# Optimization experiments

Measured on AMD Instinct MI355X. Metric: run time of the kernel, lower is better.

## Reference

```python
import jax, jax.numpy as jnp
import numpy as np

SEQ, BSZ = 512, 128
VOC, EMB, HDIM = 50000, 128, 256
TAGS = 7
BOS, EOS, PAD = 4, 5, 6
H = HDIM // 2  # per-direction hidden size
NEG = -10000.0


def setup_inputs() -> dict:
    key = jax.random.key(0)
    ks = jax.random.split(key, 12)
    s = 0.08  # ~ pytorch default init scale for these sizes
    trans = jax.random.normal(ks[10], (TAGS, TAGS), dtype=jnp.float32)
    # constraints applied in __init__: no transition FROM BOS targets / INTO EOS etc.
    trans = trans.at[BOS, :].set(NEG).at[:, EOS].set(NEG).at[PAD, :].set(0.0)
    return {
        "sen": jax.random.randint(ks[0], (SEQ, BSZ), 0, VOC),                # (S, B) token ids
        "emb": jax.random.normal(ks[1], (VOC, EMB), jnp.float32) * s,        # embedding table
        "Wih_f": jax.random.normal(ks[2], (4 * H, EMB), jnp.float32) * s,    # fwd dir, gates i,f,g,o
        "Whh_f": jax.random.normal(ks[3], (4 * H, H), jnp.float32) * s,
        "b_f": jax.random.normal(ks[4], (4 * H,), jnp.float32) * s,          # b_ih + b_hh fused
        "Wih_b": jax.random.normal(ks[5], (4 * H, EMB), jnp.float32) * s,    # bwd dir
        "Whh_b": jax.random.normal(ks[6], (4 * H, H), jnp.float32) * s,
        "b_b": jax.random.normal(ks[7], (4 * H,), jnp.float32) * s,
        "W_out": jax.random.normal(ks[8], (TAGS, HDIM), jnp.float32) * s,    # hid2tag
        "b_out": jax.random.normal(ks[9], (TAGS,), jnp.float32) * s,
        "trans": trans,                                                      # trans[next, prev]
    }


def _lstm_dir(x, Wih, Whh, b, reverse):
    """Single-direction LSTM over (S, B, E) -> (S, B, H). PyTorch gate order i,f,g,o."""
    xw = jnp.einsum('sbe,ge->sbg', x, Wih) + b  # hoist input projection out of scan

    def step(carry, xt):
        h, c = carry
        g = xt + h @ Whh.T
        i, f, gg, o = jnp.split(g, 4, axis=-1)
        c = jax.nn.sigmoid(f) * c + jax.nn.sigmoid(i) * jnp.tanh(gg)
        h = jax.nn.sigmoid(o) * jnp.tanh(c)
        return (h, c), h

    B = x.shape[1]
    h0 = jnp.zeros((B, H), x.dtype)
    _, hs = jax.lax.scan(step, (h0, h0), xw, reverse=reverse)
    return hs


def reference(sen, emb, Wih_f, Whh_f, b_f, Wih_b, Whh_b, b_b, W_out, b_out, trans):
    # ----- BiLSTM features -----
    x = emb[sen]                                   # (S, B, E)
    hf = _lstm_dir(x, Wih_f, Whh_f, b_f, reverse=False)
    hb = _lstm_dir(x, Wih_b, Whh_b, b_b, reverse=True)
    fts = jnp.concatenate([hf, hb], axis=-1) @ W_out.T + b_out   # (S, B, TAGS)

    # ----- Viterbi decode (batched, one scan over sequence) -----
    B = fts.shape[1]
    fv0 = jnp.full((B, TAGS), NEG, dtype=fts.dtype).at[:, BOS].set(0.0)

    def vstep(fv, ft):
        # scores[b, next, prev] = fv[b, prev] + trans[next, prev]
        scores = fv[:, None, :] + trans[None, :, :]
        bptr = jnp.argmax(scores, axis=2)          # (B, TAGS) best prev per next tag
        fv_new = jnp.max(scores, axis=2) + ft
        return fv_new, bptr

    fv, bptrs = jax.lax.scan(vstep, fv0, fts)      # bptrs: (S, B, TAGS)
    terminal = fv + trans[EOS]                     # (B, TAGS)
    best = jnp.argmax(terminal, axis=1)            # (B,)
    path_score = jnp.take_along_axis(terminal, best[:, None], axis=1)[:, 0]

    def bstep(cur, bptr):
        prev = jnp.take_along_axis(bptr, cur[:, None], axis=1)[:, 0]
        return prev, cur                           # output = tag at this position

    _, tag_seq = jax.lax.scan(bstep, best, bptrs, reverse=True)  # (S, B)
    return path_score, tag_seq
```

## Files before the change

### kernel.cpp

```cpp
#include <hip/hip_runtime.h>
#include <hip/hip_bf16.h>
#include <math.h>

#define SEQ  512
#define BSZ  128
#define EMBD 128
#define H4   512
#define HD   128
#define NTAG 7
#define BOSX 4
#define EOSX 5
#define NEGC (-10000.0f)

typedef _Float16 h2 __attribute__((ext_vector_type(2)));
typedef _Float16 f16x8 __attribute__((ext_vector_type(8)));
typedef float    f32x4 __attribute__((ext_vector_type(4)));

__device__ __forceinline__ float frcp(float x) { return __builtin_amdgcn_rcpf(x); }

__device__ __forceinline__ float fdot2(h2 a, h2 b, float c) {
#if __has_builtin(__builtin_amdgcn_fdot2)
    return __builtin_amdgcn_fdot2(a, b, c, false);
#else
    return c + (float)a.x * (float)b.x + (float)a.y * (float)b.y;
#endif
}

template<int C> __device__ __forceinline__ float dppaddf(float x) {
    const int y = __builtin_amdgcn_update_dpp(0, __builtin_bit_cast(int, x), C, 0xF, 0xF, true);
    return x + __builtin_bit_cast(float, y);
}
template<int C> __device__ __forceinline__ float dppmovf(float x) {
    return __builtin_bit_cast(float,
        __builtin_amdgcn_update_dpp(0, __builtin_bit_cast(int, x), C, 0xF, 0xF, true));
}
template<int C> __device__ __forceinline__ int dppmovi(int x) {
    return __builtin_amdgcn_update_dpp(0, x, C, 0xF, 0xF, true);
}
__device__ __forceinline__ float kreduce4(float x) {
    x = dppaddf<0xB1>(x);
    x = dppaddf<0x4E>(x);
    return x;
}

#define CH_DW  20
#define ROW_DW 80

__device__ __forceinline__ float dot32h(const h2* __restrict__ w, const h2* __restrict__ x) {
    float a = 0.f;
    #pragma unroll
    for (int j = 0; j < 16; ++j) a = fdot2(w[j], x[j], a);
    return a;
}
__device__ __forceinline__ void ldwh(h2* w, const float4* wr) {
    #pragma unroll
    for (int j = 0; j < 8; ++j) {
        const float4 f4 = wr[j];
        h2 a; a.x = (_Float16)f4.x; a.y = (_Float16)f4.y;
        h2 b; b.x = (_Float16)f4.z; b.y = (_Float16)f4.w;
        w[2 * j] = a; w[2 * j + 1] = b;
    }
}
__device__ __forceinline__ void unp16(const uint4* p, h2* x) {
    #pragma unroll
    for (int j = 0; j < 4; ++j) {
        x[4 * j]     = __builtin_bit_cast(h2, p[j].x);
        x[4 * j + 1] = __builtin_bit_cast(h2, p[j].y);
        x[4 * j + 2] = __builtin_bit_cast(h2, p[j].z);
        x[4 * j + 3] = __builtin_bit_cast(h2, p[j].w);
    }
}

__global__ __launch_bounds__(512) __attribute__((amdgpu_waves_per_eu(1, 2)))
void bilstm_fused(const int* __restrict__ sen, const float* __restrict__ emb,
                  const float* __restrict__ Wih_f, const float* __restrict__ b_f,
                  const float* __restrict__ Wih_b, const float* __restrict__ b_b,
                  const float* __restrict__ Whh_f, const float* __restrict__ Whh_b,
                  const float* __restrict__ W_out,
                  float* __restrict__ eft, float* __restrict__ ebt)
{
    const int tid = threadIdx.x;
    const int wid = tid >> 6;
    const int lane = tid & 63;
    const int k = lane & 3;
    const int m = lane >> 2;
    const int u = wid * 16 + m;
    const bool bk0 = (lane & 1) != 0;
    const bool bk1 = (lane & 2) != 0;
    const int col = lane & 15;
    const int kg  = lane >> 4;
    const int chain = blockIdx.x;
    const int dir = chain & 1;
    const int b = chain >> 1;
    const int t0 = dir ? (SEQ - 1) : 0;
    const int ts = dir ? -1 : 1;

    __shared__ __align__(16) _Float16 xA[2][4][4][16][8];
    __shared__ __align__(16) float zb[2][8][512];
    __shared__ __align__(16) unsigned hdb_u[2 * ROW_DW];

    const float* __restrict__ Wih  = dir ? Wih_b : Wih_f;
    const float* __restrict__ Whh  = dir ? Whh_b : Whh_f;
    const float* __restrict__ bias = dir ? b_b  : b_f;

    h2 whh[4][16], wo[16];
    #pragma unroll
    for (int g = 0; g < 4; ++g)
        ldwh(whh[g], (const float4*)(Whh + (g * HD + u) * HD + k * 32));
    {
        const int mm = (m < NTAG) ? m : 0;
        ldwh(wo, (const float4*)(W_out + mm * 256 + dir * HD + k * 32));
    }
    f16x8 bw[4][4];
    float biasv[4];
    #pragma unroll
    for (int tt = 0; tt < 4; ++tt) {
        const int R = (wid * 4 + tt) * 16 + col;
        const int ug = R >> 2;
        const int gg = R & 3;
        #pragma unroll
        for (int ks = 0; ks < 4; ++ks) {
            const float* src = Wih + (gg * HD + ug) * EMBD + ks * 32 + kg * 8;
            f16x8 v;
            #pragma unroll
            for (int j = 0; j < 8; ++j) v[j] = (_Float16)src[j];
            bw[tt][ks] = v;
        }
        biasv[tt] = bias[gg * HD + ug];
    }

    if (tid < 2 * ROW_DW) hdb_u[tid] = 0u;
    {
        unsigned* p = (unsigned*)xA;
        p[tid] = 0u; p[tid + 512] = 0u; p[tid + 1024] = 0u; p[tid + 1536] = 0u;
    }

    const int srow = wid;
    const int sp = lane;
    float2 sv;
    auto sissue = [&](int w) {
        const int row = w * 8 + srow;
        const int tg = t0 + ts * row;
        const int tok = sen[tg * BSZ + b];
        sv = *(const float2*)(emb + (size_t)tok * EMBD + 2 * sp);
    };
    auto swrite = [&](int buf) {
        h2 t; t.x = (_Float16)sv.x; t.y = (_Float16)sv.y;
        *(unsigned*)&xA[buf][sp >> 4][(sp >> 2) & 3][srow][(sp & 3) * 2]
            = __builtin_bit_cast(unsigned, t);
    };

    auto proj = [&](int bufp, int nb) {
        f16x8 ax[4];
        #pragma unroll
        for (int ks = 0; ks < 4; ++ks)
            ax[ks] = *(const f16x8*)&xA[bufp][ks][kg][col][0];
        f32x4 acc[4];
        #pragma unroll
        for (int tt = 0; tt < 4; ++tt) { acc[tt][0]=0.f; acc[tt][1]=0.f; acc[tt][2]=0.f; acc[tt][3]=0.f; }
        #pragma unroll
        for (int ks = 0; ks < 4; ++ks)
            #pragma unroll
            for (int tt = 0; tt < 4; ++tt)
                acc[tt] = __builtin_amdgcn_mfma_f32_16x16x32_f16(ax[ks], bw[tt][ks], acc[tt], 0, 0, 0);
        if (lane < 32) {
            #pragma unroll
            for (int tt = 0; tt < 4; ++tt)
                #pragma unroll
                for (int r = 0; r < 4; ++r)
                    zb[nb][(lane >> 4) * 4 + r][wid * 64 + tt * 16 + col]
                        = acc[tt][r] + biasv[tt];
        }
    };

    float c = 0.0f, v0 = 0.0f, v1 = 0.0f, v2 = 0.0f, v3 = 0.0f;
    float* __restrict__ eX = (dir ? ebt : eft) + (size_t)b * (SEQ * 8);

    sissue(0); swrite(0);
    sissue(1); swrite(1);
    __syncthreads();
    proj(0, 0);
    sissue(2);
    __syncthreads();

    for (int base = 0; base < SEQ; base += 8) {
        const int W = base >> 3;
        #pragma unroll
        for (int sl = 0; sl < 8; ++sl) {
            const int s = base + sl;
            const int cur = sl & 1;
            uint4 hpk[4];
            {
                const uint4* hr = (const uint4*)(hdb_u + cur * ROW_DW + k * CH_DW);
                #pragma unroll
                for (int j = 0; j < 4; ++j) hpk[j] = hr[j];
            }
            if (sl == 0) {
                if (base <= SEQ - 24) swrite(W & 1);
                if (base <= SEQ - 32) sissue(W + 3);
                if (W < 63) proj((W & 1) ^ 1, (W & 1) ^ 1);
            }
            const float xq = zb[W & 1][sl][wid * 64 + lane];
            h2 hx[16];
            unp16(hpk, hx);
            {
                const float pi = dot32h(whh[0], hx);
                const float pf = dot32h(whh[1], hx);
                const float pg = dot32h(whh[2], hx);
                const float po = dot32h(whh[3], hx);
                const float A = (bk0 ? pf : pi) + dppmovf<0xB1>(bk0 ? pi : pf);
                const float B = (bk0 ? po : pg) + dppmovf<0x4E>(bk0 ? pg : po);
                float z = (bk1 ? B : A) + dppmovf<0x4E>(bk1 ? A : B);
                z += xq;
                const bool isg = bk1 && !bk0;
                const float x2 = isg ? (z + z) : z;
                float y = frcp(1.0f + __expf(-x2));
                y = isg ? (2.0f * y - 1.0f) : y;
                const float r1 = dppmovf<0xB1>(y);
                const float r2 = dppmovf<0x4E>(y);
                const float r3 = dppmovf<0x4E>(r1);
                const float i0 = bk0 ? r1 : y,  i1 = bk0 ? y : r1;
                const float i2 = bk0 ? r3 : r2, i3 = bk0 ? r2 : r3;
                const float gi = bk1 ? i2 : i0;
                const float gf = bk1 ? i3 : i1;
                const float gg2 = bk1 ? i0 : i2;
                const float go = bk1 ? i1 : i3;
                c = gf * c + gi * gg2;
                const float th = 2.0f * frcp(1.0f + __expf(-2.0f * c)) - 1.0f;
                const float h = go * th;
                if (k == 0) {
                    ((unsigned short*)hdb_u)[((cur ^ 1) * ROW_DW + (u >> 5) * CH_DW) * 2 + (u & 31)]
                        = __builtin_bit_cast(unsigned short, (_Float16)h);
                }
            }
            if (wid == 0 && s >= 1) {
                const float ev = kreduce4(dot32h(wo, hx));
                const int e = s - 1;
                const bool mine = (e & 3) == k;
                const int j = (e >> 2) & 3;
                v0 = (mine && j == 0) ? ev : v0;
                v1 = (mine && j == 1) ? ev : v1;
                v2 = (mine && j == 2) ? ev : v2;
                v3 = (mine && j == 3) ? ev : v3;
                if ((s & 15) == 0 && m < NTAG) {
                    const int eA = s - 16 + k;
                    eX[(t0 + ts * (eA +  0)) * 8 + m] = v0;
                    eX[(t0 + ts * (eA +  4)) * 8 + m] = v1;
                    eX[(t0 + ts * (eA +  8)) * 8 + m] = v2;
                    eX[(t0 + ts * (eA + 12)) * 8 + m] = v3;
                }
            }
            __syncthreads();
        }
    }

    {
        h2 hx[16];
        const uint4* hr = (const uint4*)(hdb_u + k * CH_DW);
        uint4 pk[4];
        #pragma unroll
        for (int j = 0; j < 4; ++j) pk[j] = hr[j];
        unp16(pk, hx);
        if (wid == 0) {
            const float ev = kreduce4(dot32h(wo, hx));
            if (k == 3) v3 = ev;
            if (m < NTAG) {
                const int eA = SEQ - 16 + k;
                eX[(t0 + ts * (eA +  0)) * 8 + m] = v0;
                eX[(t0 + ts * (eA +  4)) * 8 + m] = v1;
                eX[(t0 + ts * (eA +  8)) * 8 + m] = v2;
                eX[(t0 + ts * (eA + 12)) * 8 + m] = v3;
            }
        }
    }
}

__global__ __launch_bounds__(256, 1)
void vit_kernel(const float* __restrict__ eft, const float* __restrict__ ebt,
                const float* __restrict__ b_out, const float* __restrict__ trans,
                float* __restrict__ out)
{
    const int b = blockIdx.x;
    const int tid = threadIdx.x;
    __shared__ __align__(16) float ftl[SEQ * 8];
    __shared__ unsigned wordL[SEQ];

    {
        const float4* sf = (const float4*)(eft + (size_t)b * (SEQ * 8));
        const float4* sb = (const float4*)(ebt + (size_t)b * (SEQ * 8));
        float4* dst = (float4*)ftl;
        #pragma unroll
        for (int i = 0; i < SEQ * 2 / 256; ++i) {
            const int idx = tid + i * 256;
            float4 a = sf[idx];
            const float4 c4 = sb[idx];
            a.x += c4.x; a.y += c4.y; a.z += c4.z; a.w += c4.w;
            dst[idx] = a;
        }
    }
    __syncthreads();

    if (tid < 64) {
        const int lane = tid;
        const int next = lane >> 3;
        const int prev = lane & 7;
        const bool pv = (prev < NTAG);
        const bool nv = (next < NTAG);
        const float trv = (pv && nv) ? (trans[next * NTAG + prev] + b_out[next]) : -3.0e38f;
        float fvp = pv ? ((prev == BOSX) ? 0.0f : NEGC) : -3.0e38f;

        for (int t = 0; t < SEQ; ++t) {
            float mv = fvp + trv;
            int am = prev;
            {
                const float om = dppmovf<0xB1>(mv); const int oa = dppmovi<0xB1>(am);
                if (om > mv || (om == mv && oa < am)) { mv = om; am = oa; }
            }
            {
                const float om = dppmovf<0x4E>(mv); const int oa = dppmovi<0x4E>(am);
                if (om > mv || (om == mv && oa < am)) { mv = om; am = oa; }
            }
            {
                const float om = dppmovf<0x141>(mv); const int oa = dppmovi<0x141>(am);
                if (om > mv || (om == mv && oa < am)) { mv = om; am = oa; }
            }
            const float fvnew = mv + ftl[t * 8 + next];
            const float nfv = __shfl(fvnew, (lane & 7) << 3);
            const int   amg = __shfl(am,    (lane & 7) << 3);
            unsigned pw = (unsigned)amg << (3 * prev);
            pw |= (unsigned)dppmovi<0xB1>((int)pw);
            pw |= (unsigned)dppmovi<0x4E>((int)pw);
            pw |= (unsigned)dppmovi<0x141>((int)pw);
            if (lane == 0) wordL[t] = pw;
            fvp = pv ? nfv : -3.0e38f;
        }

        float term = pv ? (fvp + trans[EOSX * NTAG + prev]) : -3.0e38f;
        int am = prev;
        {
            const float om = dppmovf<0xB1>(term); const int oa = dppmovi<0xB1>(am);
            if (om > term || (om == term && oa < am)) { term = om; am = oa; }
        }
        {
            const float om = dppmovf<0x4E>(term); const int oa = dppmovi<0x4E>(am);
            if (om > term || (om == term && oa < am)) { term = om; am = oa; }
        }
        {
            const float om = dppmovf<0x141>(term); const int oa = dppmovi<0x141>(am);
            if (om > term || (om == term && oa < am)) { term = om; am = oa; }
        }
        if (lane == 0) out[b] = term;

        unsigned wd[8];
        #pragma unroll
        for (int c2 = 0; c2 < 8; ++c2) wd[c2] = wordL[c2 * 64 + lane];
        int cur = __builtin_amdgcn_readfirstlane(am);
        unsigned pr[8];
        #pragma unroll
        for (int c2 = 7; c2 >= 0; --c2) {
            unsigned acc = 0u;
            for (int tt = 63; tt >= 0; --tt) {
                acc = (lane == tt) ? (unsigned)cur : acc;
                const unsigned w = (unsigned)__builtin_amdgcn_readlane((int)wd[c2], tt);
                cur = (int)((w >> (3 * cur)) & 7u);
            }
            pr[c2] = acc;
        }
        #pragma unroll
        for (int c2 = 0; c2 < 8; ++c2)
            out[BSZ + (c2 * 64 + lane) * BSZ + b] = (float)pr[c2];
    }
}

extern "C" void kernel_launch(void* const* d_in, const int* in_sizes, int n_in,
                              void* d_out, int out_size, void* d_ws, size_t ws_size,
                              hipStream_t stream)
{
    const int*   sen   = (const int*)d_in[0];
    const float* emb   = (const float*)d_in[1];
    const float* Wih_f = (const float*)d_in[2];
    const float* Whh_f = (const float*)d_in[3];
    const float* b_f   = (const float*)d_in[4];
    const float* Wih_b = (const float*)d_in[5];
    const float* Whh_b = (const float*)d_in[6];
    const float* b_b   = (const float*)d_in[7];
    const float* W_out = (const float*)d_in[8];
    const float* b_out = (const float*)d_in[9];
    const float* trans = (const float*)d_in[10];
    float* out = (float*)d_out;

    char* ws = (char*)d_ws;
    const size_t ft_bytes = (size_t)BSZ * SEQ * 8 * 4;
    float* eft = (float*)ws;
    float* ebt = (float*)(ws + ft_bytes);

    bilstm_fused<<<dim3(2 * BSZ), dim3(512), 0, stream>>>(
        sen, emb, Wih_f, b_f, Wih_b, b_b, Whh_f, Whh_b, W_out, eft, ebt);
    vit_kernel<<<dim3(BSZ), dim3(256), 0, stream>>>(eft, ebt, b_out, trans, out);
}
```

Before: 554.8 us.

## Compute LSTM recurrent matvec and emission projection with MFMA instead of fdot2

The per-step h·Whh product moves from per-lane packed fp16 dot products with DPP reductions to 16x16x32 fp16 MFMA. The weights are held as B fragments in the same layout as the input projection, and h is broadcast as the A operand. The tag emission projection also becomes an MFMA on wave 7, and each step's emission is written directly instead of buffered over 16 steps. The aim is to cut the VALU instruction count and cross-lane reduction latency on the serial recurrence. The cost is that 15 of the 16 MFMA rows are redundant, and the critical path now depends on dependent MFMA latency.

```diff
diff --git a/kernel.cpp b/kernel.cpp
--- a/kernel.cpp
+++ b/kernel.cpp
@@ -18,57 +18,12 @@
 
 __device__ __forceinline__ float frcp(float x) { return __builtin_amdgcn_rcpf(x); }
 
-__device__ __forceinline__ float fdot2(h2 a, h2 b, float c) {
-#if __has_builtin(__builtin_amdgcn_fdot2)
-    return __builtin_amdgcn_fdot2(a, b, c, false);
-#else
-    return c + (float)a.x * (float)b.x + (float)a.y * (float)b.y;
-#endif
-}
-
-template<int C> __device__ __forceinline__ float dppaddf(float x) {
-    const int y = __builtin_amdgcn_update_dpp(0, __builtin_bit_cast(int, x), C, 0xF, 0xF, true);
-    return x + __builtin_bit_cast(float, y);
-}
 template<int C> __device__ __forceinline__ float dppmovf(float x) {
     return __builtin_bit_cast(float,
         __builtin_amdgcn_update_dpp(0, __builtin_bit_cast(int, x), C, 0xF, 0xF, true));
 }
 template<int C> __device__ __forceinline__ int dppmovi(int x) {
     return __builtin_amdgcn_update_dpp(0, x, C, 0xF, 0xF, true);
-}
-__device__ __forceinline__ float kreduce4(float x) {
-    x = dppaddf<0xB1>(x);
-    x = dppaddf<0x4E>(x);
-    return x;
-}
-
-#define CH_DW  20
-#define ROW_DW 80
-
-__device__ __forceinline__ float dot32h(const h2* __restrict__ w, const h2* __restrict__ x) {
-    float a = 0.f;
-    #pragma unroll
-    for (int j = 0; j < 16; ++j) a = fdot2(w[j], x[j], a);
-    return a;
-}
-__device__ __forceinline__ void ldwh(h2* w, const float4* wr) {
-    #pragma unroll
-    for (int j = 0; j < 8; ++j) {
-        const float4 f4 = wr[j];
-        h2 a; a.x = (_Float16)f4.x; a.y = (_Float16)f4.y;
-        h2 b; b.x = (_Float16)f4.z; b.y = (_Float16)f4.w;
-        w[2 * j] = a; w[2 * j + 1] = b;
-    }
-}
-__device__ __forceinline__ void unp16(const uint4* p, h2* x) {
-    #pragma unroll
-    for (int j = 0; j < 4; ++j) {
-        x[4 * j]     = __builtin_bit_cast(h2, p[j].x);
-        x[4 * j + 1] = __builtin_bit_cast(h2, p[j].y);
-        x[4 * j + 2] = __builtin_bit_cast(h2, p[j].z);
-        x[4 * j + 3] = __builtin_bit_cast(h2, p[j].w);
-    }
 }
 
 __global__ __launch_bounds__(512) __attribute__((amdgpu_waves_per_eu(1, 2)))
@@ -82,13 +37,10 @@
     const int tid = threadIdx.x;
     const int wid = tid >> 6;
     const int lane = tid & 63;
-    const int k = lane & 3;
-    const int m = lane >> 2;
-    const int u = wid * 16 + m;
+    const int col = lane & 15;
+    const int kg  = lane >> 4;
     const bool bk0 = (lane & 1) != 0;
     const bool bk1 = (lane & 2) != 0;
-    const int col = lane & 15;
-    const int kg  = lane >> 4;
     const int chain = blockIdx.x;
     const int dir = chain & 1;
     const int b = chain >> 1;
@@ -97,21 +49,13 @@
 
     __shared__ __align__(16) _Float16 xA[2][4][4][16][8];
     __shared__ __align__(16) float zb[2][8][512];
-    __shared__ __align__(16) unsigned hdb_u[2 * ROW_DW];
+    __shared__ __align__(16) _Float16 hA[2][128];
 
     const float* __restrict__ Wih  = dir ? Wih_b : Wih_f;
     const float* __restrict__ Whh  = dir ? Whh_b : Whh_f;
     const float* __restrict__ bias = dir ? b_b  : b_f;
 
-    h2 whh[4][16], wo[16];
-    #pragma unroll
-    for (int g = 0; g < 4; ++g)
-        ldwh(whh[g], (const float4*)(Whh + (g * HD + u) * HD + k * 32));
-    {
-        const int mm = (m < NTAG) ? m : 0;
-        ldwh(wo, (const float4*)(W_out + mm * 256 + dir * HD + k * 32));
-    }
-    f16x8 bw[4][4];
+    f16x8 bw[4][4], bwh[4][4], be[4];
     float biasv[4];
     #pragma unroll
     for (int tt = 0; tt < 4; ++tt) {
@@ -120,16 +64,26 @@
         const int gg = R & 3;
         #pragma unroll
         for (int ks = 0; ks < 4; ++ks) {
-            const float* src = Wih + (gg * HD + ug) * EMBD + ks * 32 + kg * 8;
-            f16x8 v;
-            #pragma unroll
-            for (int j = 0; j < 8; ++j) v[j] = (_Float16)src[j];
-            bw[tt][ks] = v;
+            const float* s1 = Wih + (gg * HD + ug) * EMBD + ks * 32 + kg * 8;
+            const float* s2 = Whh + (gg * HD + ug) * HD   + ks * 32 + kg * 8;
+            f16x8 v1, v2;
+            #pragma unroll
+            for (int j = 0; j < 8; ++j) { v1[j] = (_Float16)s1[j]; v2[j] = (_Float16)s2[j]; }
+            bw[tt][ks] = v1; bwh[tt][ks] = v2;
         }
         biasv[tt] = bias[gg * HD + ug];
     }
-
-    if (tid < 2 * ROW_DW) hdb_u[tid] = 0u;
+    #pragma unroll
+    for (int ks = 0; ks < 4; ++ks) {
+        f16x8 v;
+        #pragma unroll
+        for (int j = 0; j < 8; ++j)
+            v[j] = (col < NTAG) ? (_Float16)W_out[col * 256 + dir * HD + ks * 32 + kg * 8 + j]
+                                : (_Float16)0.f;
+        be[ks] = v;
+    }
+
+    if (tid < 256) ((_Float16*)hA)[tid] = (_Float16)0.f;
     {
         unsigned* p = (unsigned*)xA;
         p[tid] = 0u; p[tid + 512] = 0u; p[tid + 1024] = 0u; p[tid + 1536] = 0u;
@@ -173,7 +127,7 @@
         }
     };
 
-    float c = 0.0f, v0 = 0.0f, v1 = 0.0f, v2 = 0.0f, v3 = 0.0f;
+    float c = 0.0f;
     float* __restrict__ eX = (dir ? ebt : eft) + (size_t)b * (SEQ * 8);
 
     sissue(0); swrite(0);
@@ -189,89 +143,68 @@
         for (int sl = 0; sl < 8; ++sl) {
             const int s = base + sl;
             const int cur = sl & 1;
-            uint4 hpk[4];
-            {
-                const uint4* hr = (const uint4*)(hdb_u + cur * ROW_DW + k * CH_DW);
-                #pragma unroll
-                for (int j = 0; j < 4; ++j) hpk[j] = hr[j];
-            }
+            f16x8 ah[4];
+            #pragma unroll
+            for (int ks = 0; ks < 4; ++ks)
+                ah[ks] = *(const f16x8*)&hA[cur][ks * 32 + kg * 8];
             if (sl == 0) {
                 if (base <= SEQ - 24) swrite(W & 1);
                 if (base <= SEQ - 32) sissue(W + 3);
                 if (W < 63) proj((W & 1) ^ 1, (W & 1) ^ 1);
             }
-            const float xq = zb[W & 1][sl][wid * 64 + lane];
-            h2 hx[16];
-            unp16(hpk, hx);
-            {
-                const float pi = dot32h(whh[0], hx);
-                const float pf = dot32h(whh[1], hx);
-                const float pg = dot32h(whh[2], hx);
-                const float po = dot32h(whh[3], hx);
-                const float A = (bk0 ? pf : pi) + dppmovf<0xB1>(bk0 ? pi : pf);
-                const float B = (bk0 ? po : pg) + dppmovf<0x4E>(bk0 ? pg : po);
-                float z = (bk1 ? B : A) + dppmovf<0x4E>(bk1 ? A : B);
-                z += xq;
-                const bool isg = bk1 && !bk0;
+            f32x4 acc[4];
+            #pragma unroll
+            for (int tt = 0; tt < 4; ++tt) { acc[tt][0]=0.f; acc[tt][1]=0.f; acc[tt][2]=0.f; acc[tt][3]=0.f; }
+            #pragma unroll
+            for (int ks = 0; ks < 4; ++ks)
+                #pragma unroll
+                for (int tt = 0; tt < 4; ++tt)
+                    acc[tt] = __builtin_amdgcn_mfma_f32_16x16x32_f16(ah[ks], bwh[tt][ks], acc[tt], 0, 0, 0);
+            f32x4 eacc; eacc[0]=0.f; eacc[1]=0.f; eacc[2]=0.f; eacc[3]=0.f;
+            if (wid == 7 && s >= 1) {
+                #pragma unroll
+                for (int ks = 0; ks < 4; ++ks)
+                    eacc = __builtin_amdgcn_mfma_f32_16x16x32_f16(ah[ks], be[ks], eacc, 0, 0, 0);
+            }
+            const bool isg = bk1 && !bk0;
+            float y[4];
+            #pragma unroll
+            for (int tt = 0; tt < 4; ++tt) {
+                const float z = acc[tt][0] + zb[W & 1][sl][wid * 64 + tt * 16 + col];
                 const float x2 = isg ? (z + z) : z;
-                float y = frcp(1.0f + __expf(-x2));
-                y = isg ? (2.0f * y - 1.0f) : y;
-                const float r1 = dppmovf<0xB1>(y);
-                const float r2 = dppmovf<0x4E>(y);
-                const float r3 = dppmovf<0x4E>(r1);
-                const float i0 = bk0 ? r1 : y,  i1 = bk0 ? y : r1;
-                const float i2 = bk0 ? r3 : r2, i3 = bk0 ? r2 : r3;
-                const float gi = bk1 ? i2 : i0;
-                const float gf = bk1 ? i3 : i1;
-                const float gg2 = bk1 ? i0 : i2;
-                const float go = bk1 ? i1 : i3;
-                c = gf * c + gi * gg2;
-                const float th = 2.0f * frcp(1.0f + __expf(-2.0f * c)) - 1.0f;
-                const float h = go * th;
-                if (k == 0) {
-                    ((unsigned short*)hdb_u)[((cur ^ 1) * ROW_DW + (u >> 5) * CH_DW) * 2 + (u & 31)]
-                        = __builtin_bit_cast(unsigned short, (_Float16)h);
-                }
-            }
-            if (wid == 0 && s >= 1) {
-                const float ev = kreduce4(dot32h(wo, hx));
-                const int e = s - 1;
-                const bool mine = (e & 3) == k;
-                const int j = (e >> 2) & 3;
-                v0 = (mine && j == 0) ? ev : v0;
-                v1 = (mine && j == 1) ? ev : v1;
-                v2 = (mine && j == 2) ? ev : v2;
-                v3 = (mine && j == 3) ? ev : v3;
-                if ((s & 15) == 0 && m < NTAG) {
-                    const int eA = s - 16 + k;
-                    eX[(t0 + ts * (eA +  0)) * 8 + m] = v0;
-                    eX[(t0 + ts * (eA +  4)) * 8 + m] = v1;
-                    eX[(t0 + ts * (eA +  8)) * 8 + m] = v2;
-                    eX[(t0 + ts * (eA + 12)) * 8 + m] = v3;
-                }
-            }
+                const float yy = frcp(1.0f + __expf(-x2));
+                y[tt] = isg ? (2.0f * yy - 1.0f) : yy;
+            }
+            const float n0 = bk0 ? dppmovf<0xB1>(y[1]) : y[0];
+            const float n1 = bk0 ? y[1] : dppmovf<0xB1>(y[0]);
+            const float n2 = bk0 ? dppmovf<0xB1>(y[3]) : y[2];
+            const float n3 = bk0 ? y[3] : dppmovf<0xB1>(y[2]);
+            const float m0 = bk1 ? dppmovf<0x4E>(n2) : n0;
+            const float m2 = bk1 ? n2 : dppmovf<0x4E>(n0);
+            const float m1 = bk1 ? dppmovf<0x4E>(n3) : n1;
+            const float m3 = bk1 ? n3 : dppmovf<0x4E>(n1);
+            c = m1 * c + m0 * m2;
+            const float th = 2.0f * frcp(1.0f + __expf(-2.0f * c)) - 1.0f;
+            const float h = m3 * th;
+            if (kg == 0)
+                hA[cur ^ 1][wid * 16 + (lane & 3) * 4 + (lane >> 2)] = (_Float16)h;
+            if (wid == 7 && s >= 1 && kg == 0 && col < NTAG)
+                eX[(t0 + ts * (s - 1)) * 8 + col] = eacc[0];
             __syncthreads();
         }
     }
 
-    {
-        h2 hx[16];
-        const uint4* hr = (const uint4*)(hdb_u + k * CH_DW);
-        uint4 pk[4];
-        #pragma unroll
-        for (int j = 0; j < 4; ++j) pk[j] = hr[j];
-        unp16(pk, hx);
-        if (wid == 0) {
-            const float ev = kreduce4(dot32h(wo, hx));
-            if (k == 3) v3 = ev;
-            if (m < NTAG) {
-                const int eA = SEQ - 16 + k;
-                eX[(t0 + ts * (eA +  0)) * 8 + m] = v0;
-                eX[(t0 + ts * (eA +  4)) * 8 + m] = v1;
-                eX[(t0 + ts * (eA +  8)) * 8 + m] = v2;
-                eX[(t0 + ts * (eA + 12)) * 8 + m] = v3;
-            }
-        }
+    if (wid == 7) {
+        f16x8 ah[4];
+        #pragma unroll
+        for (int ks = 0; ks < 4; ++ks)
+            ah[ks] = *(const f16x8*)&hA[0][ks * 32 + kg * 8];
+        f32x4 eacc; eacc[0]=0.f; eacc[1]=0.f; eacc[2]=0.f; eacc[3]=0.f;
+        #pragma unroll
+        for (int ks = 0; ks < 4; ++ks)
+            eacc = __builtin_amdgcn_mfma_f32_16x16x32_f16(ah[ks], be[ks], eacc, 0, 0, 0);
+        if (kg == 0 && col < NTAG)
+            eX[(t0 + ts * (SEQ - 1)) * 8 + col] = eacc[0];
     }
 }
 
```

Result: slower. 597.4 us (+7.7%).
